# Kernel tuning notes

Hardware: AMD Instinct MI355X
Metric: run time of the kernel (lower is better)

Reference implementation:

```python
import jax, jax.numpy as jnp
import numpy as np


def setup_inputs() -> dict:
    key = jax.random.key(0)
    ks = jax.random.split(key, 8)
    B, Cin, Cattr, Cout, H, W = 8, 256, 256, 256, 64, 64
    x = jax.random.normal(ks[0], (B, Cin, H, W), dtype=jnp.float32)
    attr = jax.random.normal(ks[1], (B, Cattr, H, W), dtype=jnp.float32)
    # 1x1 conv weights stored as [out, in] (kernel_size=1 squeezed)
    sq = 1.0 / np.sqrt(Cin)
    sa = 1.0 / np.sqrt(Cattr)
    Wq = jax.random.uniform(ks[2], (Cout, Cin), jnp.float32, -sq, sq)
    bq = jax.random.uniform(ks[3], (Cout,), jnp.float32, -sq, sq)
    Wk = jax.random.uniform(ks[4], (Cout, Cattr), jnp.float32, -sa, sa)
    bk = jax.random.uniform(ks[5], (Cout,), jnp.float32, -sa, sa)
    Wv = jax.random.uniform(ks[6], (Cout, Cattr), jnp.float32, -sa, sa)
    bv = jax.random.uniform(ks[7], (Cout,), jnp.float32, -sa, sa)
    return {"x": x, "attr": attr, "Wq": Wq, "bq": bq, "Wk": Wk, "bk": bk, "Wv": Wv, "bv": bv}


def reference(x, attr, Wq, bq, Wk, bk, Wv, bv):
    B, Cin, H, W = x.shape
    # 1x1 convs == per-pixel linear projections
    q = jnp.einsum('bchw,oc->bohw', x, Wq) + bq[None, :, None, None]      # [B,C,H,W]
    k = jnp.einsum('bchw,oc->bohw', attr, Wk) + bk[None, :, None, None]
    v = jnp.einsum('bchw,oc->bohw', attr, Wv) + bv[None, :, None, None]
    C = q.shape[1]
    qf = q.reshape(B, C, H * W)   # [B,C,N]
    kf = k.reshape(B, C, H * W)
    vf = v.reshape(B, C, H * W)
    # attn[b,i,j] = sum_c q[b,c,i] * k[b,c,j]  -> softmax over j
    attn = jax.nn.softmax(jnp.einsum('bci,bcj->bij', qf, kf), axis=-1)    # [B,N,N]
    out = jnp.einsum('bcj,bij->bci', vf, attn)                            # [B,C,N]
    return out.reshape(B, C, H, W) + x
```

## Files before the change

kernel.cpp:

```cpp
#include <hip/hip_runtime.h>

typedef _Float16 f16;
typedef _Float16 f16x8 __attribute__((ext_vector_type(8)));
typedef _Float16 f16x4 __attribute__((ext_vector_type(4)));
typedef float f32x4 __attribute__((ext_vector_type(4)));
typedef float f32x16 __attribute__((ext_vector_type(16)));

#define LOG2E 1.44269504088896340736f
#define SOFF  36.0f
#define CDIM 256
#define NPIX 4096

__device__ __forceinline__ void gl2lds16(const f16* g, const f16* l) {
    __builtin_amdgcn_global_load_lds((const __attribute__((address_space(1))) unsigned int*)g,
                                     (__attribute__((address_space(3))) unsigned int*)l, 16, 0, 0);
}

__global__ void convert_w_kernel(const float* __restrict__ Wq, const float* __restrict__ Wk,
                                 const float* __restrict__ Wv,
                                 f16* __restrict__ WqF, f16* __restrict__ WkF,
                                 f16* __restrict__ WvF) {
    int t = blockIdx.x * 256 + threadIdx.x;
    int m = t >> 13;
    int g = t & 8191;
    int lane = g & 63;
    int ksct = g >> 6;
    int ks = ksct & 15, ct = ksct >> 4;
    int o = ct * 32 + (lane & 31);
    int cin0 = ks * 16 + (lane >> 5) * 8;
    const float* W = (m == 0) ? Wq : ((m == 1) ? Wk : Wv);
    f16* WF = (m == 0) ? WqF : ((m == 1) ? WkF : WvF);
    const float scale = (m == 0) ? LOG2E : 1.0f;
    const float* src = W + (size_t)o * CDIM + cin0;
    f16x8 v;
#pragma unroll
    for (int e = 0; e < 8; ++e) v[e] = (f16)(src[e] * scale);
    *(f16x8*)(WF + (size_t)g * 8) = v;
}

__global__ __launch_bounds__(256, 2)
void proj_kernel(const float* __restrict__ x, const float* __restrict__ attr,
                 const f16* __restrict__ WqF, const float* __restrict__ bq,
                 const f16* __restrict__ WkF, const float* __restrict__ bk,
                 const f16* __restrict__ WvF, const float* __restrict__ bv,
                 f16* __restrict__ qT, f16* __restrict__ kC, f16* __restrict__ vW) {
    __shared__ __align__(16) f16 Xs[64 * 256];
    __shared__ __align__(16) f16 As[64 * 256];
    __shared__ __align__(16) f16 Ostage[4][1024];

    const int b  = blockIdx.x & 7;
    const int i0 = (blockIdx.x >> 3) * 64;
    const int t  = threadIdx.x;
    const int w = t >> 6, lane = t & 63, l31 = lane & 31, hi = lane >> 5;
    const int xu  = (l31 >> 1) & 15;
    const int hib = (hi ^ (l31 & 1)) * 8;

    {
        const int i  = t & 63;
        const int cb = t >> 6;
        const float* xb = x    + (size_t)b * CDIM * NPIX + i0 + i;
        const float* ab = attr + (size_t)b * CDIM * NPIX + i0 + i;
#pragma unroll 2
        for (int rep = 0; rep < 8; ++rep) {
            int chunk = cb * 8 + rep;
            const float* xs = xb + (size_t)(chunk * 8) * NPIX;
            const float* as_ = ab + (size_t)(chunk * 8) * NPIX;
            f16x8 xv, av;
#pragma unroll
            for (int e = 0; e < 8; ++e) {
                xv[e] = (f16)xs[(size_t)e * NPIX];
                av[e] = (f16)as_[(size_t)e * NPIX];
            }
            int phys = chunk ^ (i & 31);
            *(f16x8*)(Xs + i * 256 + phys * 8) = xv;
            *(f16x8*)(As + i * 256 + phys * 8) = av;
        }
    }
    __syncthreads();

#pragma unroll 1
    for (int k = 0; k < 12; ++k) {
        const int tt = w + 4 * k;
        const int kind = tt >> 4;
        const int rr = tt & 15;
        const int ct = rr >> 1;
        const int half = rr & 1;

        const f16* WF = (kind == 0) ? WqF : ((kind == 1) ? WkF : WvF);
        const f16* Bs = (kind == 0) ? Xs : As;
        const float* bias = (kind == 0) ? bq : ((kind == 1) ? bk : bv);
        const float bscale = (kind == 0) ? LOG2E : 1.0f;

        const f16* ap = WF + (size_t)(ct * 16) * 512 + (size_t)lane * 8;
        const f16* bp = Bs + (half * 32 + l31) * 256 + hib;

        f32x16 ae, ao;
#pragma unroll
        for (int r = 0; r < 16; ++r) { ae[r] = 0.0f; ao[r] = 0.0f; }
#pragma unroll
        for (int h2 = 0; h2 < 8; ++h2) {
            f16x8 a0 = *(const f16x8*)(ap + (2 * h2) * 512);
            f16x8 a1 = *(const f16x8*)(ap + (2 * h2 + 1) * 512);
            f16x8 b0 = *(const f16x8*)(bp + (((2 * h2) ^ xu)) * 16);
            f16x8 b1 = *(const f16x8*)(bp + (((2 * h2 + 1) ^ xu)) * 16);
            ae = __builtin_amdgcn_mfma_f32_32x32x16_f16(a0, b0, ae, 0, 0, 0);
            ao = __builtin_amdgcn_mfma_f32_32x32x16_f16(a1, b1, ao, 0, 0, 0);
        }

        f16* st = Ostage[w];
        if (kind < 2) {
#pragma unroll
            for (int g = 0; g < 4; ++g) {
                f32x4 bb = *(const f32x4*)(bias + ct * 32 + 4 * hi + 8 * g);
                f16x4 pk;
#pragma unroll
                for (int e = 0; e < 4; ++e)
                    pk[e] = (f16)(ae[4 * g + e] + ao[4 * g + e] + bb[e] * bscale);
                *(f16x4*)(st + l31 * 32 + 4 * hi + 8 * g) = pk;
            }
            if (kind == 0) {
                f16* dst = qT + ((size_t)b * NPIX + i0 + half * 32) * CDIM + ct * 32;
#pragma unroll
                for (int d = 0; d < 2; ++d) {
                    int row = d * 16 + (lane >> 2);
                    int c8  = (lane & 3) * 8;
                    f16x8 v = *(const f16x8*)(st + row * 32 + c8);
                    *(f16x8*)(dst + (size_t)row * CDIM + c8) = v;
                }
            } else {
                const int j0 = i0 + half * 32;
                f16* dstb = kC + (size_t)b * CDIM * NPIX;
#pragma unroll
                for (int d = 0; d < 2; ++d) {
                    int row = d * 16 + (lane >> 2);
                    int kl  = lane & 3;
                    f16x8 v = *(const f16x8*)(st + row * 32 + kl * 8);
                    *(f16x8*)(dstb + ((size_t)(ct * 4 + kl) * NPIX + j0 + row) * 8) = v;
                }
            }
        } else {
#pragma unroll
            for (int g = 0; g < 4; ++g) {
                f32x4 bb = *(const f32x4*)(bias + ct * 32 + 4 * hi + 8 * g);
#pragma unroll
                for (int e = 0; e < 4; ++e) {
                    int c31 = 4 * hi + 8 * g + e;
                    st[c31 * 32 + l31] = (f16)(ae[4 * g + e] + ao[4 * g + e] + bb[e]);
                }
            }
            const int j0 = i0 + half * 32;
            f16* dstb = vW + (size_t)b * CDIM * NPIX + (size_t)(ct * 32) * NPIX + j0;
#pragma unroll
            for (int d = 0; d < 2; ++d) {
                int chunk = d * 64 + lane;
                int c31 = chunk >> 2, jch = chunk & 3;
                *(f16x8*)(dstb + (size_t)c31 * NPIX + jch * 8) =
                    *(const f16x8*)(st + chunk * 8);
            }
        }
    }
}

__global__ __launch_bounds__(512, 2)
void attn_kernel(const f16* __restrict__ qT, const f16* __restrict__ kC,
                 const f16* __restrict__ vW, const float* __restrict__ x,
                 float* __restrict__ out) {
    extern __shared__ unsigned char smem[];

    const int b    = blockIdx.x & 7;
    const int i0   = (blockIdx.x >> 3) * 128;
    const int t    = threadIdx.x;
    const int w    = t >> 6;
    const int lane = t & 63;
    const int l31  = lane & 31;
    const int hi   = lane >> 5;
    const int iw   = (w & 3) * 32;
    const int jh   = (w >> 2) * 32;
    const int jh8  = (w >> 2) * 4;
    const int ig   = i0 + iw + l31;

    f16x8 qf[16];
    {
        const f16* qp = qT + ((size_t)b * NPIX + ig) * CDIM + hi * 8;
#pragma unroll
        for (int ks = 0; ks < 16; ++ks) qf[ks] = *(const f16x8*)(qp + ks * 16);
    }

    const int kbase = hi * 512 + (jh >> 5) * 256 + l31 * 8;
    int vp2o[2];
    {
        int vbase = 16384 + (l31 & 7) * 256 + ((l31 >> 3) << 6);
#pragma unroll
        for (int kj = 0; kj < 2; ++kj)
            vp2o[kj] = vbase + (((jh8 + 2 * kj + hi) ^ (l31 & 7)) << 3);
    }

    f32x16 acc[8];
#pragma unroll
    for (int ct = 0; ct < 8; ++ct)
#pragma unroll
        for (int r = 0; r < 16; ++r) acc[ct][r] = 0.0f;
    float lrun = 0.0f;

    const f16* kb = kC + (size_t)b * CDIM * NPIX;
    const f16* vb = vW + (size_t)b * CDIM * NPIX;
    f16* lds0 = (f16*)smem;
    const int wub = (t & ~63) * 8;

    {
#pragma unroll
        for (int rep = 0; rep < 4; ++rep) {
            int slot = t + rep * 512;
            int kc = slot >> 6, jhalf = (slot >> 5) & 1, pj = slot & 31;
            gl2lds16(kb + ((size_t)kc * NPIX + jhalf * 32 + pj) * 8,
                     lds0 + wub + rep * 4096);
            int row = slot >> 5, pv = slot & 31;
            int vc = ((row >> 3) << 5) | (((pv >> 3) & 3) << 3) | (row & 7);
            int vjc = (pv & 7) ^ (row & 7);
            gl2lds16(vb + (size_t)vc * NPIX + vjc * 8,
                     lds0 + 16384 + wub + rep * 4096);
        }
    }

    union Q4 { f16x4 h; unsigned int u[2]; };
    union B8 { f16x8 h; unsigned int u[4]; };

#pragma unroll 1
    for (int jt = 0; jt < 64; ++jt) {
        const int p = jt & 1;
        __syncthreads();

        if (jt < 63) {
            const int j0n = (jt + 1) * 64;
            f16* dstb = lds0 + (p ^ 1) * 32768;
#pragma unroll
            for (int rep = 0; rep < 4; ++rep) {
                int slot = t + rep * 512;
                int kc = slot >> 6, jhalf = (slot >> 5) & 1, pj = slot & 31;
                gl2lds16(kb + ((size_t)kc * NPIX + j0n + jhalf * 32 + pj) * 8,
                         dstb + wub + rep * 4096);
                int row = slot >> 5, pv = slot & 31;
                int vc = ((row >> 3) << 5) | (((pv >> 3) & 3) << 3) | (row & 7);
                int vjc = (pv & 7) ^ (row & 7);
                gl2lds16(vb + (size_t)vc * NPIX + j0n + vjc * 8,
                         dstb + 16384 + wub + rep * 4096);
            }
        }

        const f16* L = lds0 + p * 32768;

        f32x16 s;
#pragma unroll
        for (int r = 0; r < 16; ++r) s[r] = -SOFF;
#pragma unroll
        for (int ks = 0; ks < 16; ++ks)
            s = __builtin_amdgcn_mfma_f32_32x32x16_f16(
                *(const f16x8*)(L + kbase + ks * 1024), qf[ks], s, 0, 0, 0);

        Q4 ownq[4];
        float rtot = 0.0f;
#pragma unroll
        for (int g = 0; g < 4; ++g) {
            float p0 = __builtin_amdgcn_exp2f(s[4 * g + 0]);
            float p1 = __builtin_amdgcn_exp2f(s[4 * g + 1]);
            float p2 = __builtin_amdgcn_exp2f(s[4 * g + 2]);
            float p3 = __builtin_amdgcn_exp2f(s[4 * g + 3]);
            rtot += (p0 + p1) + (p2 + p3);
            ownq[g].h[0] = (f16)p0; ownq[g].h[1] = (f16)p1;
            ownq[g].h[2] = (f16)p2; ownq[g].h[3] = (f16)p3;
        }
        lrun += rtot;

        f16x8 pb[2];
#pragma unroll
        for (int kj = 0; kj < 2; ++kj) {
            int sidx = 2 * kj + 1 - hi;
            int oidx = 2 * kj + hi;
            unsigned int s0 = ownq[sidx].u[0], s1 = ownq[sidx].u[1];
            unsigned int r0 = (unsigned int)__shfl_xor((int)s0, 32);
            unsigned int r1 = (unsigned int)__shfl_xor((int)s1, 32);
            B8 bb;
            bb.u[0] = hi ? r0 : ownq[oidx].u[0];
            bb.u[1] = hi ? r1 : ownq[oidx].u[1];
            bb.u[2] = hi ? ownq[oidx].u[0] : r0;
            bb.u[3] = hi ? ownq[oidx].u[1] : r1;
            pb[kj] = bb.h;
        }

#pragma unroll
        for (int ct = 0; ct < 8; ++ct) {
            acc[ct] = __builtin_amdgcn_mfma_f32_32x32x16_f16(
                *(const f16x8*)(L + vp2o[0] + ct * 2048), pb[0], acc[ct], 0, 0, 0);
            acc[ct] = __builtin_amdgcn_mfma_f32_32x32x16_f16(
                *(const f16x8*)(L + vp2o[1] + ct * 2048), pb[1], acc[ct], 0, 0, 0);
        }
    }

    float lsum = lrun + __shfl_xor(lrun, 32);
    __syncthreads();
    float* Obuf = (float*)smem;
    float* Ls   = (float*)(smem + 131072);
    if (w >= 4) {
        float* ob = Obuf + (w - 4) * 8192;
#pragma unroll
        for (int ct = 0; ct < 8; ++ct)
#pragma unroll
            for (int r = 0; r < 16; ++r) {
                int c = ct * 32 + (r & 3) + 8 * (r >> 2) + 4 * hi;
                ob[c * 32 + l31] = acc[ct][r];
            }
        if (hi == 0) Ls[(w - 4) * 32 + l31] = lsum;
    }
    __syncthreads();
    if (w < 4) {
        const float ltot = lsum + Ls[w * 32 + l31];
        const float invl = 1.0f / ltot;
        const float* po = Obuf + w * 8192;
        const float* xb = x + (size_t)b * CDIM * NPIX + i0 + iw;
        float* og = out + (size_t)b * CDIM * NPIX + i0 + iw;
#pragma unroll
        for (int ct = 0; ct < 8; ++ct)
#pragma unroll
            for (int r = 0; r < 16; ++r) {
                int c = ct * 32 + (r & 3) + 8 * (r >> 2) + 4 * hi;
                size_t off = (size_t)c * NPIX + l31;
                og[off] = (acc[ct][r] + po[c * 32 + l31]) * invl + xb[off];
            }
    }
}

extern "C" void kernel_launch(void* const* d_in, const int* in_sizes, int n_in,
                              void* d_out, int out_size, void* d_ws, size_t ws_size,
                              hipStream_t stream) {
    const float* x    = (const float*)d_in[0];
    const float* attr = (const float*)d_in[1];
    const float* Wq   = (const float*)d_in[2];
    const float* bq   = (const float*)d_in[3];
    const float* Wk   = (const float*)d_in[4];
    const float* bk   = (const float*)d_in[5];
    const float* Wv   = (const float*)d_in[6];
    const float* bv   = (const float*)d_in[7];
    float* out = (float*)d_out;

    char* ws = (char*)d_ws;
    const size_t qkv_bytes = (size_t)8 * NPIX * CDIM * sizeof(f16);
    f16* qT   = (f16*)ws;
    f16* kC   = (f16*)(ws + qkv_bytes);
    f16* vW   = (f16*)(ws + 2 * qkv_bytes);
    f16* WqF  = (f16*)(ws + 3 * qkv_bytes);
    f16* WkF  = WqF + 65536;
    f16* WvF  = WkF + 65536;

    (void)hipFuncSetAttribute((const void*)attn_kernel,
                              hipFuncAttributeMaxDynamicSharedMemorySize, 131584);

    convert_w_kernel<<<96, 256, 0, stream>>>(Wq, Wk, Wv, WqF, WkF, WvF);
    proj_kernel<<<512, 256, 0, stream>>>(x, attr, WqF, bq, WkF, bk, WvF, bv, qT, kC, vW);
    attn_kernel<<<256, 512, 131584, stream>>>(qT, kC, vW, x, out);
}
```

Baseline: 298.0 us.

## Software-pipeline PV of previous tile with QK of current tile via LDS-shared P

Restructures the attention loop so each wave's QK^T MFMAs for tile j are interleaved with the PV MFMAs for tile j-1, and V is loaded one tile later than K. P is exchanged through LDS so the two j-half waves each own half the output channels, rather than each computing all channels over half the keys. This removes the cross-wave output reduction through LDS at the end and halves accumulator registers. In exchange it adds an extra barrier per iteration, LDS traffic for P, and more shared memory per block, which may reduce occupancy.

```diff
diff --git a/kernel.cpp b/kernel.cpp
--- a/kernel.cpp
+++ b/kernel.cpp
@@ -167,17 +167,17 @@
                  float* __restrict__ out) {
     extern __shared__ unsigned char smem[];
 
-    const int b    = blockIdx.x & 7;
-    const int i0   = (blockIdx.x >> 3) * 128;
-    const int t    = threadIdx.x;
-    const int w    = t >> 6;
-    const int lane = t & 63;
-    const int l31  = lane & 31;
-    const int hi   = lane >> 5;
-    const int iw   = (w & 3) * 32;
-    const int jh   = (w >> 2) * 32;
-    const int jh8  = (w >> 2) * 4;
-    const int ig   = i0 + iw + l31;
+    const int b     = blockIdx.x & 7;
+    const int i0    = (blockIdx.x >> 3) * 128;
+    const int t     = threadIdx.x;
+    const int w     = t >> 6;
+    const int lane  = t & 63;
+    const int l31   = lane & 31;
+    const int hi    = lane >> 5;
+    const int pr    = w & 3;
+    const int chalf = w >> 2;
+    const int jh    = chalf * 32;
+    const int ig    = i0 + pr * 32 + l31;
 
     f16x8 qf[16];
     {
@@ -186,18 +186,18 @@
         for (int ks = 0; ks < 16; ++ks) qf[ks] = *(const f16x8*)(qp + ks * 16);
     }
 
-    const int kbase = hi * 512 + (jh >> 5) * 256 + l31 * 8;
-    int vp2o[2];
+    const int kbase = hi * 512 + chalf * 256 + l31 * 8;
+    int vp4o[4];
     {
         int vbase = 16384 + (l31 & 7) * 256 + ((l31 >> 3) << 6);
 #pragma unroll
-        for (int kj = 0; kj < 2; ++kj)
-            vp2o[kj] = vbase + (((jh8 + 2 * kj + hi) ^ (l31 & 7)) << 3);
-    }
-
-    f32x16 acc[8];
-#pragma unroll
-    for (int ct = 0; ct < 8; ++ct)
+        for (int kjg = 0; kjg < 4; ++kjg)
+            vp4o[kjg] = vbase + (((2 * kjg + hi) ^ (l31 & 7)) << 3);
+    }
+
+    f32x16 acc[4];
+#pragma unroll
+    for (int ct = 0; ct < 4; ++ct)
 #pragma unroll
         for (int r = 0; r < 16; ++r) acc[ct][r] = 0.0f;
     float lrun = 0.0f;
@@ -205,6 +205,7 @@
     const f16* kb = kC + (size_t)b * CDIM * NPIX;
     const f16* vb = vW + (size_t)b * CDIM * NPIX;
     f16* lds0 = (f16*)smem;
+    f16* Pb   = lds0 + 65536 + pr * 2048;
     const int wub = (t & ~63) * 8;
 
     {
@@ -214,11 +215,6 @@
             int kc = slot >> 6, jhalf = (slot >> 5) & 1, pj = slot & 31;
             gl2lds16(kb + ((size_t)kc * NPIX + jhalf * 32 + pj) * 8,
                      lds0 + wub + rep * 4096);
-            int row = slot >> 5, pv = slot & 31;
-            int vc = ((row >> 3) << 5) | (((pv >> 3) & 3) << 3) | (row & 7);
-            int vjc = (pv & 7) ^ (row & 7);
-            gl2lds16(vb + (size_t)vc * NPIX + vjc * 8,
-                     lds0 + 16384 + wub + rep * 4096);
         }
     }
 
@@ -230,32 +226,51 @@
         const int p = jt & 1;
         __syncthreads();
 
-        if (jt < 63) {
+        {
+            f16* kdst = lds0 + (p ^ 1) * 32768 + wub;
+            f16* vdst = lds0 + p * 32768 + 16384 + wub;
             const int j0n = (jt + 1) * 64;
-            f16* dstb = lds0 + (p ^ 1) * 32768;
+            const int j0v = jt * 64;
 #pragma unroll
             for (int rep = 0; rep < 4; ++rep) {
                 int slot = t + rep * 512;
-                int kc = slot >> 6, jhalf = (slot >> 5) & 1, pj = slot & 31;
-                gl2lds16(kb + ((size_t)kc * NPIX + j0n + jhalf * 32 + pj) * 8,
-                         dstb + wub + rep * 4096);
+                if (jt < 63) {
+                    int kc = slot >> 6, jhalf = (slot >> 5) & 1, pj = slot & 31;
+                    gl2lds16(kb + ((size_t)kc * NPIX + j0n + jhalf * 32 + pj) * 8,
+                             kdst + rep * 4096);
+                }
                 int row = slot >> 5, pv = slot & 31;
                 int vc = ((row >> 3) << 5) | (((pv >> 3) & 3) << 3) | (row & 7);
                 int vjc = (pv & 7) ^ (row & 7);
-                gl2lds16(vb + (size_t)vc * NPIX + j0n + vjc * 8,
-                         dstb + 16384 + wub + rep * 4096);
-            }
-        }
-
-        const f16* L = lds0 + p * 32768;
+                gl2lds16(vb + (size_t)vc * NPIX + j0v + vjc * 8,
+                         vdst + rep * 4096);
+            }
+        }
+
+        const f16* Lk = lds0 + p * 32768;
+        const f16* Lv = lds0 + (p ^ 1) * 32768;
 
         f32x16 s;
 #pragma unroll
         for (int r = 0; r < 16; ++r) s[r] = -SOFF;
-#pragma unroll
-        for (int ks = 0; ks < 16; ++ks)
-            s = __builtin_amdgcn_mfma_f32_32x32x16_f16(
-                *(const f16x8*)(L + kbase + ks * 1024), qf[ks], s, 0, 0, 0);
+        if (jt > 0) {
+            f16x8 pf;
+#pragma unroll
+            for (int u = 0; u < 16; ++u) {
+                const int kjg = u >> 2, ctl = u & 3;
+                if ((u & 3) == 0) pf = *(const f16x8*)(Pb + kjg * 512 + lane * 8);
+                s = __builtin_amdgcn_mfma_f32_32x32x16_f16(
+                    *(const f16x8*)(Lk + kbase + u * 1024), qf[u], s, 0, 0, 0);
+                acc[ctl] = __builtin_amdgcn_mfma_f32_32x32x16_f16(
+                    *(const f16x8*)(Lv + vp4o[kjg] + (chalf * 4 + ctl) * 2048),
+                    pf, acc[ctl], 0, 0, 0);
+            }
+        } else {
+#pragma unroll
+            for (int ks = 0; ks < 16; ++ks)
+                s = __builtin_amdgcn_mfma_f32_32x32x16_f16(
+                    *(const f16x8*)(Lk + kbase + ks * 1024), qf[ks], s, 0, 0, 0);
+        }
 
         Q4 ownq[4];
         float rtot = 0.0f;
@@ -287,46 +302,41 @@
             pb[kj] = bb.h;
         }
 
-#pragma unroll
-        for (int ct = 0; ct < 8; ++ct) {
-            acc[ct] = __builtin_amdgcn_mfma_f32_32x32x16_f16(
-                *(const f16x8*)(L + vp2o[0] + ct * 2048), pb[0], acc[ct], 0, 0, 0);
-            acc[ct] = __builtin_amdgcn_mfma_f32_32x32x16_f16(
-                *(const f16x8*)(L + vp2o[1] + ct * 2048), pb[1], acc[ct], 0, 0, 0);
+        __syncthreads();
+        *(f16x8*)(Pb + (chalf * 2 + 0) * 512 + lane * 8) = pb[0];
+        *(f16x8*)(Pb + (chalf * 2 + 1) * 512 + lane * 8) = pb[1];
+    }
+
+    __syncthreads();
+    {
+        const f16* Lv = lds0 + 32768;
+#pragma unroll
+        for (int kjg = 0; kjg < 4; ++kjg) {
+            f16x8 pf = *(const f16x8*)(Pb + kjg * 512 + lane * 8);
+#pragma unroll
+            for (int ctl = 0; ctl < 4; ++ctl)
+                acc[ctl] = __builtin_amdgcn_mfma_f32_32x32x16_f16(
+                    *(const f16x8*)(Lv + vp4o[kjg] + (chalf * 4 + ctl) * 2048),
+                    pf, acc[ctl], 0, 0, 0);
         }
     }
 
     float lsum = lrun + __shfl_xor(lrun, 32);
+    float* Lsm = (float*)(smem + 147456);
+    if (hi == 0) Lsm[w * 32 + l31] = lsum;
     __syncthreads();
-    float* Obuf = (float*)smem;
-    float* Ls   = (float*)(smem + 131072);
-    if (w >= 4) {
-        float* ob = Obuf + (w - 4) * 8192;
-#pragma unroll
-        for (int ct = 0; ct < 8; ++ct)
-#pragma unroll
-            for (int r = 0; r < 16; ++r) {
-                int c = ct * 32 + (r & 3) + 8 * (r >> 2) + 4 * hi;
-                ob[c * 32 + l31] = acc[ct][r];
-            }
-        if (hi == 0) Ls[(w - 4) * 32 + l31] = lsum;
-    }
-    __syncthreads();
-    if (w < 4) {
-        const float ltot = lsum + Ls[w * 32 + l31];
-        const float invl = 1.0f / ltot;
-        const float* po = Obuf + w * 8192;
-        const float* xb = x + (size_t)b * CDIM * NPIX + i0 + iw;
-        float* og = out + (size_t)b * CDIM * NPIX + i0 + iw;
-#pragma unroll
-        for (int ct = 0; ct < 8; ++ct)
-#pragma unroll
-            for (int r = 0; r < 16; ++r) {
-                int c = ct * 32 + (r & 3) + 8 * (r >> 2) + 4 * hi;
-                size_t off = (size_t)c * NPIX + l31;
-                og[off] = (acc[ct][r] + po[c * 32 + l31]) * invl + xb[off];
-            }
-    }
+    const float ltot = lsum + Lsm[(w ^ 4) * 32 + l31];
+    const float invl = 1.0f / ltot;
+    const float* xb = x + (size_t)b * CDIM * NPIX;
+    float* og = out + (size_t)b * CDIM * NPIX;
+#pragma unroll
+    for (int ctl = 0; ctl < 4; ++ctl)
+#pragma unroll
+        for (int r = 0; r < 16; ++r) {
+            int c = (chalf * 4 + ctl) * 32 + (r & 3) + 8 * (r >> 2) + 4 * hi;
+            size_t off = (size_t)c * NPIX + ig;
+            og[off] = acc[ctl][r] * invl + xb[off];
+        }
 }
 
 extern "C" void kernel_launch(void* const* d_in, const int* in_sizes, int n_in,
@@ -352,9 +362,9 @@
     f16* WvF  = WkF + 65536;
 
     (void)hipFuncSetAttribute((const void*)attn_kernel,
-                              hipFuncAttributeMaxDynamicSharedMemorySize, 131584);
+                              hipFuncAttributeMaxDynamicSharedMemorySize, 148480);
 
     convert_w_kernel<<<96, 256, 0, stream>>>(Wq, Wk, Wv, WqF, WkF, WvF);
     proj_kernel<<<512, 256, 0, stream>>>(x, attr, WqF, bq, WkF, bk, WvF, bv, qT, kC, vW);
-    attn_kernel<<<256, 512, 131584, stream>>>(qT, kC, vW, x, out);
-}
+    attn_kernel<<<256, 512, 148480, stream>>>(qT, kC, vW, x, out);
+}
```

New measurement: 361.8 us. 21.4% more time.
